# Kernel optimization log

Hardware: AMD Instinct MI355X
Metric: run time of the kernel (lower is better)

Reference implementation:

```python
import jax, jax.numpy as jnp
import numpy as np

PATCH = 16
EMBED = 384
BINS = 32
LN_EPS = 1e-5


def setup_inputs() -> dict:
    key = jax.random.key(0)
    k1, k2 = jax.random.split(key, 2)
    images = jax.random.uniform(k1, (64, 3, 224, 224), dtype=jnp.float32)  # pixels in [0,1]
    proj_w = jax.random.normal(k2, (EMBED, 3, PATCH, PATCH), dtype=jnp.float32) * 0.02  # OIHW
    proj_b = jnp.zeros((EMBED,), jnp.float32)
    ln_gamma = jnp.ones((EMBED,), jnp.float32)
    ln_beta = jnp.zeros((EMBED,), jnp.float32)
    return {"images": images, "proj_w": proj_w, "proj_b": proj_b,
            "ln_gamma": ln_gamma, "ln_beta": ln_beta}


def _patch_entropy(images, patch_size):
    # images: (B, C, H, W) in [0,1]
    B, C, H, W = images.shape
    gH, gW = H // patch_size, W // patch_size
    gray = images.mean(axis=1)  # (B, H, W)
    # non-overlapping patches -> (B, N, P*P)
    patches = gray.reshape(B, gH, patch_size, gW, patch_size)
    patches = patches.transpose(0, 1, 3, 2, 4).reshape(B, gH * gW, patch_size * patch_size)
    # quantize to 32 bins (floor, matching torch .long() on non-negative values)
    q = jnp.clip(patches * (BINS - 1), 0, BINS - 1).astype(jnp.int32)
    one_hot = jax.nn.one_hot(q, BINS, dtype=jnp.float32)      # (B, N, P*P, 32)
    hist = one_hot.sum(axis=2)                                 # (B, N, 32)
    prob = hist / jnp.maximum(hist.sum(axis=-1, keepdims=True), 1e-8)
    log_prob = jnp.log2(prob + 1e-10)
    entropy = -(prob * log_prob).sum(axis=-1)                  # (B, N)
    return entropy / np.float32(np.log2(BINS))


def reference(images, proj_w, proj_b, ln_gamma, ln_beta):
    p = PATCH
    B, C, H, W = images.shape
    gH, gW = H // p, W // p
    entropy = _patch_entropy(images, p)
    # patch-embed conv: kernel=stride=patch_size, VALID padding
    x = jax.lax.conv_general_dilated(
        images, proj_w, window_strides=(p, p), padding='VALID',
        dimension_numbers=('NCHW', 'OIHW', 'NCHW'))            # (B, D, gH, gW)
    x = x + proj_b[None, :, None, None]
    x = x.transpose(0, 2, 3, 1).reshape(B, gH * gW, -1)        # (B, N, D)
    mu = x.mean(axis=-1, keepdims=True)
    var = x.var(axis=-1, keepdims=True)                        # biased, like torch LayerNorm
    x = (x - mu) / jnp.sqrt(var + LN_EPS) * ln_gamma + ln_beta
    return x, entropy
```

## Files before the change

kernel.cpp:

```cpp
#include <hip/hip_runtime.h>

#define BATCH 64
#define GH 14
#define GW 14
#define NPATCH (GH*GW)
#define M_ROWS (BATCH*NPATCH)
#define KDIM 768
#define DDIM 384
#define HW (224*224)

typedef __attribute__((ext_vector_type(8))) short s16x8;
typedef __attribute__((ext_vector_type(4))) float f32x4;
typedef __attribute__((ext_vector_type(4))) unsigned short u16x4;

__device__ __forceinline__ unsigned short f2bf(float f) {
    unsigned int u = __float_as_uint(f);
    u += 0x7fff + ((u >> 16) & 1);
    return (unsigned short)(u >> 16);
}

__device__ __forceinline__ s16x8 cvt8(float4 lo, float4 hi) {
    s16x8 o;
    o[0] = (short)f2bf(lo.x); o[1] = (short)f2bf(lo.y);
    o[2] = (short)f2bf(lo.z); o[3] = (short)f2bf(lo.w);
    o[4] = (short)f2bf(hi.x); o[5] = (short)f2bf(hi.y);
    o[6] = (short)f2bf(hi.z); o[7] = (short)f2bf(hi.w);
    return o;
}

__global__ __launch_bounds__(256) void wcast_kernel(const float* __restrict__ w,
                                                    unsigned short* __restrict__ W) {
    int t = blockIdx.x * 256 + threadIdx.x;
    float4 v = ((const float4*)w)[t];
    u16x4 o = { f2bf(v.x), f2bf(v.y), f2bf(v.z), f2bf(v.w) };
    *(u16x4*)(W + t * 4) = o;
}

__global__ __launch_bounds__(384, 2) void fused_kernel(const float* __restrict__ img,
                                                       const unsigned short* __restrict__ Bt,
                                                       const float* __restrict__ bias,
                                                       const float* __restrict__ gamma,
                                                       const float* __restrict__ beta,
                                                       float* __restrict__ C,
                                                       float* __restrict__ ent) {
    __shared__ __align__(16) unsigned short As0[32 * 64];
    __shared__ __align__(16) unsigned short As1[32 * 64];
    __shared__ int hist[6][32];
    __shared__ float sred[32], sred2[32], smean[32], srstd[32];

    const int tid  = threadIdx.x;
    const int lane = tid & 63;
    const int wv   = tid >> 6;
    const int quad = lane >> 4;
    const int cl   = lane & 15;
    const int rowBase = blockIdx.x * 32;

    if (tid < 32) { sred[tid] = 0.0f; sred2[tid] = 0.0f; }

    const int r1  = tid >> 3, ksg = tid & 7;
    const int sA1 = r1 * 64 + (ksg ^ (r1 & 7)) * 8;
    const float* pA1;
    {
        int p = rowBase + r1, b = p / NPATCH, n = p - b * NPATCH;
        int ph = n / GW, pw_ = n - ph * GW;
        pA1 = img + (size_t)b * (3 * HW) + (ph * 16 + (ksg >> 1)) * 224 + pw_ * 16 + (ksg & 1) * 8;
    }
    const unsigned short* pBr = Bt + (size_t)(wv * 64 + cl) * KDIM + quad * 8;

    s16x8 bcur[8];
#pragma unroll
    for (int j = 0; j < 4; ++j)
#pragma unroll
        for (int ks = 0; ks < 2; ++ks)
            bcur[ks * 4 + j] = *(const s16x8*)(pBr + j * (16 * KDIM) + ks * 32);
    float4 a0lo, a0hi, aNlo, aNhi;
    if (tid < 256) {
        a0lo = *(const float4*)(pA1);
        a0hi = *(const float4*)(pA1 + 4);
        const float* p1 = pA1 + 1 * (4 * 224);
        aNlo = *(const float4*)(p1);
        aNhi = *(const float4*)(p1 + 4);
    }

    {
        const int pr  = lane >> 2;
        const int cc4 = (lane & 3) * 4;
        int p0 = rowBase + wv, b0 = p0 / NPATCH, n0i = p0 - b0 * NPATCH;
        int ph0 = n0i / GW, pw0 = n0i - ph0 * GW;
        const float* bp = img + (size_t)b0 * (3 * HW) + (ph0 * 16 + pr) * 224 + pw0 * 16 + cc4;
        float4 c0 = *(const float4*)(bp);
        float4 c1 = *(const float4*)(bp + HW);
        float4 c2 = *(const float4*)(bp + 2 * HW);
        for (int pp = wv; pp < 32; pp += 6) {
            float4 n0, n1, n2;
            if (pp + 6 < 32) {
                int p = rowBase + pp + 6, b = p / NPATCH, n = p - b * NPATCH;
                int ph = n / GW, pw_ = n - ph * GW;
                const float* np = img + (size_t)b * (3 * HW) + (ph * 16 + pr) * 224 + pw_ * 16 + cc4;
                n0 = *(const float4*)(np);
                n1 = *(const float4*)(np + HW);
                n2 = *(const float4*)(np + 2 * HW);
            }
            if (lane < 32) hist[wv][lane] = 0;
            asm volatile("s_waitcnt lgkmcnt(0)" ::: "memory");
            float g[4] = { (c0.x + c1.x + c2.x) / 3.0f, (c0.y + c1.y + c2.y) / 3.0f,
                           (c0.z + c1.z + c2.z) / 3.0f, (c0.w + c1.w + c2.w) / 3.0f };
#pragma unroll
            for (int j = 0; j < 4; ++j) {
                int bin = (int)(g[j] * 31.0f);
                bin = bin < 0 ? 0 : (bin > 31 ? 31 : bin);
                atomicAdd(&hist[wv][bin], 1);
            }
            asm volatile("s_waitcnt lgkmcnt(0)" ::: "memory");
            float t = 0.0f;
            if (lane < 32) {
                float prb = (float)hist[wv][lane] * (1.0f / 256.0f);
                t = -prb * log2f(prb + 1e-10f);
            }
#pragma unroll
            for (int off = 32; off; off >>= 1) t += __shfl_xor(t, off);
            if (lane == 0) ent[rowBase + pp] = t * (1.0f / 5.0f);
            c0 = n0; c1 = n1; c2 = n2;
        }
    }

    if (tid < 256) *(s16x8*)(As0 + sA1) = cvt8(a0lo, a0hi);
    __syncthreads();

    f32x4 acc[2][4] = {};
#pragma unroll
    for (int t = 0; t < 12; ++t) {
        unsigned short* Aw = (t & 1) ? As0 : As1;
        const unsigned short* Ar = (t & 1) ? As1 : As0;
        if (t < 11 && tid < 256)
            *(s16x8*)(Aw + sA1) = cvt8(aNlo, aNhi);
        if (t < 10 && tid < 256) {
            const int kn = t + 2;
            const float* p = pA1 + (kn >> 2) * HW + (kn & 3) * (4 * 224);
            aNlo = *(const float4*)(p);
            aNhi = *(const float4*)(p + 4);
        }
#pragma unroll
        for (int ks = 0; ks < 2; ++ks) {
            const int sw = (ks * 4 + quad) ^ (cl & 7);
            s16x8 af0 = *(const s16x8*)(Ar + (0 * 16 + cl) * 64 + sw * 8);
            s16x8 af1 = *(const s16x8*)(Ar + (1 * 16 + cl) * 64 + sw * 8);
#pragma unroll
            for (int j = 0; j < 4; ++j) {
                acc[0][j] = __builtin_amdgcn_mfma_f32_16x16x32_bf16(af0, bcur[ks * 4 + j], acc[0][j], 0, 0, 0);
                acc[1][j] = __builtin_amdgcn_mfma_f32_16x16x32_bf16(af1, bcur[ks * 4 + j], acc[1][j], 0, 0, 0);
            }
        }
        if (t < 11) {
#pragma unroll
            for (int j = 0; j < 4; ++j)
#pragma unroll
                for (int ks = 0; ks < 2; ++ks)
                    bcur[ks * 4 + j] = *(const s16x8*)(pBr + j * (16 * KDIM) + (t + 1) * 64 + ks * 32);
            __syncthreads();
        }
    }

    float bv[4], gv[4], btv[4];
#pragma unroll
    for (int j = 0; j < 4; ++j) {
        int col = wv * 64 + j * 16 + cl;
        bv[j] = bias[col]; gv[j] = gamma[col]; btv[j] = beta[col];
    }

#pragma unroll
    for (int i = 0; i < 2; ++i) {
#pragma unroll
        for (int r = 0; r < 4; ++r) {
            float s1 = 0.0f, s2 = 0.0f;
#pragma unroll
            for (int j = 0; j < 4; ++j) {
                float v = acc[i][j][r] + bv[j];
                s1 += v; s2 += v * v;
            }
#pragma unroll
            for (int off = 1; off < 16; off <<= 1) {
                s1 += __shfl_xor(s1, off);
                s2 += __shfl_xor(s2, off);
            }
            if (cl == 0) {
                int row = i * 16 + quad * 4 + r;
                atomicAdd(&sred[row], s1);
                atomicAdd(&sred2[row], s2);
            }
        }
    }
    __syncthreads();
    if (tid < 32) {
        float mu  = sred[tid] * (1.0f / (float)DDIM);
        float var = sred2[tid] * (1.0f / (float)DDIM) - mu * mu;
        smean[tid] = mu;
        srstd[tid] = rsqrtf(var + 1e-5f);
    }
    __syncthreads();

#pragma unroll
    for (int i = 0; i < 2; ++i) {
#pragma unroll
        for (int r = 0; r < 4; ++r) {
            int row = i * 16 + quad * 4 + r;
            float mu = smean[row], rs = srstd[row];
            float* crow = C + (size_t)(rowBase + row) * DDIM;
#pragma unroll
            for (int j = 0; j < 4; ++j)
                crow[wv * 64 + j * 16 + cl] = (acc[i][j][r] + bv[j] - mu) * rs * gv[j] + btv[j];
        }
    }
}

extern "C" void kernel_launch(void* const* d_in, const int* in_sizes, int n_in,
                              void* d_out, int out_size, void* d_ws, size_t ws_size,
                              hipStream_t stream) {
    const float* img = (const float*)d_in[0];
    const float* pw  = (const float*)d_in[1];
    const float* pb  = (const float*)d_in[2];
    const float* gam = (const float*)d_in[3];
    const float* bet = (const float*)d_in[4];
    float* out = (float*)d_out;

    unsigned short* Wbf = (unsigned short*)d_ws;
    float* ent = out + (size_t)M_ROWS * DDIM;

    hipLaunchKernelGGL(wcast_kernel, dim3(288), dim3(256), 0, stream, pw, Wbf);
    hipLaunchKernelGGL(fused_kernel, dim3(392), dim3(384), 0, stream,
                       img, Wbf, pb, gam, bet, out, ent);
}
```

Measured before the change: 125.7 us.

## Stage weight tiles through LDS with direct global-to-LDS loads

Projection-weight K-slices are now copied straight into a 48KB shared buffer with global_load_lds, one region per wave. Each wave reads its B fragments from LDS together with its A fragments at the start of every K step, then issues the next slice's async loads before running its MFMAs. This replaces the per-thread register prefetch of B, cutting register pressure and vector-load instructions. In exchange it adds LDS traffic and a sizeable LDS footprint, and the launch bound no longer requests two blocks per CU.

```diff
diff --git a/kernel.cpp b/kernel.cpp
--- a/kernel.cpp
+++ b/kernel.cpp
@@ -28,6 +28,12 @@
     return o;
 }
 
+__device__ __forceinline__ void load_lds16(const void* g, void* l) {
+    __builtin_amdgcn_global_load_lds(
+        (const __attribute__((address_space(1))) unsigned int*)g,
+        (__attribute__((address_space(3))) unsigned int*)l, 16, 0, 0);
+}
+
 __global__ __launch_bounds__(256) void wcast_kernel(const float* __restrict__ w,
                                                     unsigned short* __restrict__ W) {
     int t = blockIdx.x * 256 + threadIdx.x;
@@ -36,15 +42,16 @@
     *(u16x4*)(W + t * 4) = o;
 }
 
-__global__ __launch_bounds__(384, 2) void fused_kernel(const float* __restrict__ img,
-                                                       const unsigned short* __restrict__ Bt,
-                                                       const float* __restrict__ bias,
-                                                       const float* __restrict__ gamma,
-                                                       const float* __restrict__ beta,
-                                                       float* __restrict__ C,
-                                                       float* __restrict__ ent) {
+__global__ __launch_bounds__(384) void fused_kernel(const float* __restrict__ img,
+                                                    const unsigned short* __restrict__ Bt,
+                                                    const float* __restrict__ bias,
+                                                    const float* __restrict__ gamma,
+                                                    const float* __restrict__ beta,
+                                                    float* __restrict__ C,
+                                                    float* __restrict__ ent) {
     __shared__ __align__(16) unsigned short As0[32 * 64];
     __shared__ __align__(16) unsigned short As1[32 * 64];
+    __shared__ __align__(16) unsigned short Bs[384 * 64];
     __shared__ int hist[6][32];
     __shared__ float sred[32], sred2[32], smean[32], srstd[32];
 
@@ -65,14 +72,13 @@
         int ph = n / GW, pw_ = n - ph * GW;
         pA1 = img + (size_t)b * (3 * HW) + (ph * 16 + (ksg >> 1)) * 224 + pw_ * 16 + (ksg & 1) * 8;
     }
-    const unsigned short* pBr = Bt + (size_t)(wv * 64 + cl) * KDIM + quad * 8;
-
-    s16x8 bcur[8];
-#pragma unroll
-    for (int j = 0; j < 4; ++j)
-#pragma unroll
-        for (int ks = 0; ks < 2; ++ks)
-            bcur[ks * 4 + j] = *(const s16x8*)(pBr + j * (16 * KDIM) + ks * 32);
+    const int l3 = lane >> 3, l7 = lane & 7;
+    const unsigned short* pBsrc = Bt + (size_t)(wv * 64 + l3) * KDIM + ((l7 ^ l3) * 8);
+    unsigned short* ldsB = Bs + (wv * 8) * 512 + lane * 8;
+
+#pragma unroll
+    for (int i = 0; i < 8; ++i)
+        load_lds16(pBsrc + i * (8 * KDIM), ldsB + i * 512);
     float4 a0lo, a0hi, aNlo, aNhi;
     if (tid < 256) {
         a0lo = *(const float4*)(pA1);
@@ -130,10 +136,28 @@
     f32x4 acc[2][4] = {};
 #pragma unroll
     for (int t = 0; t < 12; ++t) {
+        const unsigned short* Ar = (t & 1) ? As1 : As0;
         unsigned short* Aw = (t & 1) ? As0 : As1;
-        const unsigned short* Ar = (t & 1) ? As1 : As0;
-        if (t < 11 && tid < 256)
-            *(s16x8*)(Aw + sA1) = cvt8(aNlo, aNhi);
+
+        s16x8 af[2][2], bf[2][4];
+#pragma unroll
+        for (int ks = 0; ks < 2; ++ks) {
+            const int sw = (ks * 4 + quad) ^ (cl & 7);
+            af[ks][0] = *(const s16x8*)(Ar + (0 * 16 + cl) * 64 + sw * 8);
+            af[ks][1] = *(const s16x8*)(Ar + (1 * 16 + cl) * 64 + sw * 8);
+#pragma unroll
+            for (int j = 0; j < 4; ++j)
+                bf[ks][j] = *(const s16x8*)(Bs + (wv * 64 + j * 16 + cl) * 64 + sw * 8);
+        }
+        asm volatile("s_waitcnt lgkmcnt(0)" ::: "memory");
+        __builtin_amdgcn_sched_barrier(0);
+
+        if (t < 11) {
+#pragma unroll
+            for (int i = 0; i < 8; ++i)
+                load_lds16(pBsrc + (t + 1) * 64 + i * (8 * KDIM), ldsB + i * 512);
+            if (tid < 256) *(s16x8*)(Aw + sA1) = cvt8(aNlo, aNhi);
+        }
         if (t < 10 && tid < 256) {
             const int kn = t + 2;
             const float* p = pA1 + (kn >> 2) * HW + (kn & 3) * (4 * 224);
@@ -141,24 +165,13 @@
             aNhi = *(const float4*)(p + 4);
         }
 #pragma unroll
-        for (int ks = 0; ks < 2; ++ks) {
-            const int sw = (ks * 4 + quad) ^ (cl & 7);
-            s16x8 af0 = *(const s16x8*)(Ar + (0 * 16 + cl) * 64 + sw * 8);
-            s16x8 af1 = *(const s16x8*)(Ar + (1 * 16 + cl) * 64 + sw * 8);
+        for (int ks = 0; ks < 2; ++ks)
 #pragma unroll
             for (int j = 0; j < 4; ++j) {
-                acc[0][j] = __builtin_amdgcn_mfma_f32_16x16x32_bf16(af0, bcur[ks * 4 + j], acc[0][j], 0, 0, 0);
-                acc[1][j] = __builtin_amdgcn_mfma_f32_16x16x32_bf16(af1, bcur[ks * 4 + j], acc[1][j], 0, 0, 0);
-            }
-        }
-        if (t < 11) {
-#pragma unroll
-            for (int j = 0; j < 4; ++j)
-#pragma unroll
-                for (int ks = 0; ks < 2; ++ks)
-                    bcur[ks * 4 + j] = *(const s16x8*)(pBr + j * (16 * KDIM) + (t + 1) * 64 + ks * 32);
-            __syncthreads();
-        }
+                acc[0][j] = __builtin_amdgcn_mfma_f32_16x16x32_bf16(af[ks][0], bf[ks][j], acc[0][j], 0, 0, 0);
+                acc[1][j] = __builtin_amdgcn_mfma_f32_16x16x32_bf16(af[ks][1], bf[ks][j], acc[1][j], 0, 0, 0);
+            }
+        if (t < 11) __syncthreads();
     }
 
     float bv[4], gv[4], btv[4];
```

New measurement: 124.3 us. Within noise of the previous version (-1.1%).

## Stage entire A tile in shared memory upfront and drop per-step barriers

Applied to the files above, without the earlier changes.

Replaces the double-buffered A staging, which needed a barrier every K step, with a single preload of all 12 K-slices of the 32-row A tile into a 48KB shared buffer. The main loop then runs without any __syncthreads. B fragments are now loaded from global at the top of each iteration with no register prefetch, and the loop is no longer unrolled. The occupancy hint of 2 blocks per SM is dropped. The larger LDS footprint and the loss of B prefetch may reduce occupancy and expose global load latency to the MFMAs.

```diff
diff --git a/kernel.cpp b/kernel.cpp
--- a/kernel.cpp
+++ b/kernel.cpp
@@ -36,15 +36,14 @@
     *(u16x4*)(W + t * 4) = o;
 }
 
-__global__ __launch_bounds__(384, 2) void fused_kernel(const float* __restrict__ img,
-                                                       const unsigned short* __restrict__ Bt,
-                                                       const float* __restrict__ bias,
-                                                       const float* __restrict__ gamma,
-                                                       const float* __restrict__ beta,
-                                                       float* __restrict__ C,
-                                                       float* __restrict__ ent) {
-    __shared__ __align__(16) unsigned short As0[32 * 64];
-    __shared__ __align__(16) unsigned short As1[32 * 64];
+__global__ __launch_bounds__(384) void fused_kernel(const float* __restrict__ img,
+                                                    const unsigned short* __restrict__ Bt,
+                                                    const float* __restrict__ bias,
+                                                    const float* __restrict__ gamma,
+                                                    const float* __restrict__ beta,
+                                                    float* __restrict__ C,
+                                                    float* __restrict__ ent) {
+    __shared__ __align__(16) unsigned short As[12 * 32 * 64];
     __shared__ int hist[6][32];
     __shared__ float sred[32], sred2[32], smean[32], srstd[32];
 
@@ -66,21 +65,6 @@
         pA1 = img + (size_t)b * (3 * HW) + (ph * 16 + (ksg >> 1)) * 224 + pw_ * 16 + (ksg & 1) * 8;
     }
     const unsigned short* pBr = Bt + (size_t)(wv * 64 + cl) * KDIM + quad * 8;
-
-    s16x8 bcur[8];
-#pragma unroll
-    for (int j = 0; j < 4; ++j)
-#pragma unroll
-        for (int ks = 0; ks < 2; ++ks)
-            bcur[ks * 4 + j] = *(const s16x8*)(pBr + j * (16 * KDIM) + ks * 32);
-    float4 a0lo, a0hi, aNlo, aNhi;
-    if (tid < 256) {
-        a0lo = *(const float4*)(pA1);
-        a0hi = *(const float4*)(pA1 + 4);
-        const float* p1 = pA1 + 1 * (4 * 224);
-        aNlo = *(const float4*)(p1);
-        aNhi = *(const float4*)(p1 + 4);
-    }
 
     {
         const int pr  = lane >> 2;
@@ -124,40 +108,37 @@
         }
     }
 
-    if (tid < 256) *(s16x8*)(As0 + sA1) = cvt8(a0lo, a0hi);
+    if (tid < 256) {
+#pragma unroll 4
+        for (int t = 0; t < 12; ++t) {
+            const float* p = pA1 + (t >> 2) * HW + (t & 3) * (4 * 224);
+            float4 lo = *(const float4*)(p);
+            float4 hi = *(const float4*)(p + 4);
+            *(s16x8*)(As + t * 2048 + sA1) = cvt8(lo, hi);
+        }
+    }
     __syncthreads();
 
     f32x4 acc[2][4] = {};
-#pragma unroll
+#pragma unroll 1
     for (int t = 0; t < 12; ++t) {
-        unsigned short* Aw = (t & 1) ? As0 : As1;
-        const unsigned short* Ar = (t & 1) ? As1 : As0;
-        if (t < 11 && tid < 256)
-            *(s16x8*)(Aw + sA1) = cvt8(aNlo, aNhi);
-        if (t < 10 && tid < 256) {
-            const int kn = t + 2;
-            const float* p = pA1 + (kn >> 2) * HW + (kn & 3) * (4 * 224);
-            aNlo = *(const float4*)(p);
-            aNhi = *(const float4*)(p + 4);
-        }
+        const unsigned short* At = As + t * 2048;
+        s16x8 bf[2][4];
+#pragma unroll
+        for (int ks = 0; ks < 2; ++ks)
+#pragma unroll
+            for (int j = 0; j < 4; ++j)
+                bf[ks][j] = *(const s16x8*)(pBr + j * (16 * KDIM) + t * 64 + ks * 32);
 #pragma unroll
         for (int ks = 0; ks < 2; ++ks) {
             const int sw = (ks * 4 + quad) ^ (cl & 7);
-            s16x8 af0 = *(const s16x8*)(Ar + (0 * 16 + cl) * 64 + sw * 8);
-            s16x8 af1 = *(const s16x8*)(Ar + (1 * 16 + cl) * 64 + sw * 8);
+            s16x8 af0 = *(const s16x8*)(At + (0 * 16 + cl) * 64 + sw * 8);
+            s16x8 af1 = *(const s16x8*)(At + (1 * 16 + cl) * 64 + sw * 8);
 #pragma unroll
             for (int j = 0; j < 4; ++j) {
-                acc[0][j] = __builtin_amdgcn_mfma_f32_16x16x32_bf16(af0, bcur[ks * 4 + j], acc[0][j], 0, 0, 0);
-                acc[1][j] = __builtin_amdgcn_mfma_f32_16x16x32_bf16(af1, bcur[ks * 4 + j], acc[1][j], 0, 0, 0);
-            }
-        }
-        if (t < 11) {
-#pragma unroll
-            for (int j = 0; j < 4; ++j)
-#pragma unroll
-                for (int ks = 0; ks < 2; ++ks)
-                    bcur[ks * 4 + j] = *(const s16x8*)(pBr + j * (16 * KDIM) + (t + 1) * 64 + ks * 32);
-            __syncthreads();
+                acc[0][j] = __builtin_amdgcn_mfma_f32_16x16x32_bf16(af0, bf[ks][j], acc[0][j], 0, 0, 0);
+                acc[1][j] = __builtin_amdgcn_mfma_f32_16x16x32_bf16(af1, bf[ks][j], acc[1][j], 0, 0, 0);
+            }
         }
     }
 
```

Result: slower. 130.7 us (+4.0%).
